# Kernel tuning notes

Hardware: AMD Instinct MI355X
Metric: run time of the kernel (lower is better)

## Reference

```python
import jax, jax.numpy as jnp
import numpy as np

B, C, E, S, L, N = 2, 256, 256, 3, 5, 128
HMAX = 128
LEVEL_SIZES = np.array([128, 64, 32, 16, 8])
STRIDES = np.array([8.0, 16.0, 32.0, 64.0, 128.0])
GROUPS = 8
EPS = 1e-5


def setup_inputs() -> dict:
    key = jax.random.key(0)
    ks = jax.random.split(key, 16)
    # Padded FPN pyramid stacked as [L, B, C, HMAX, HMAX]; level l valid in [:sz, :sz]
    fm = jnp.zeros((L, B, C, HMAX, HMAX), jnp.float32)
    for l in range(L):
        sz = int(LEVEL_SIZES[l])
        fm = fm.at[l, :, :, :sz, :sz].set(jax.random.normal(ks[l], (B, C, sz, sz), jnp.float32))
    # Boxes in 1024x1024 image coordinates (x1, y1, x2, y2)
    cxy = jax.random.uniform(ks[5], (N, 2), minval=60.0, maxval=960.0)
    wh = jax.random.uniform(ks[6], (N, 2), minval=8.0, maxval=96.0)
    boxes = jnp.concatenate([cxy - wh / 2, cxy + wh / 2], axis=1)
    batch_idx = jax.random.randint(ks[7], (N,), 0, B, jnp.int32)
    level_idx = jax.random.randint(ks[8], (N,), 0, L, jnp.int32)
    sym_ids = jax.random.randint(ks[9], (N,), 0, 6, jnp.int32)
    conv_w = jax.random.normal(ks[10], (E, C, 3, 3), jnp.float32) / np.float32(np.sqrt(C * 9))
    gn_scale = jnp.ones((E,), jnp.float32)
    gn_bias = jnp.zeros((E,), jnp.float32)
    head_w = jax.random.normal(ks[11], (E, E), jnp.float32) / np.float32(np.sqrt(E))
    head_b = jnp.zeros((E,), jnp.float32)
    spat_w = jax.random.normal(ks[12], (E, 4), jnp.float32) * 0.01
    spat_b = jnp.zeros((E,), jnp.float32)
    sym_emb = jax.random.normal(ks[13], (6, E), jnp.float32) * 0.05
    fuse_w = jax.random.normal(ks[14], (6, E, E), jnp.float32) / np.float32(np.sqrt(E))
    fuse_b = jnp.zeros((6, E), jnp.float32)
    return dict(feature_maps=fm, boxes=boxes, conv_w=conv_w, gn_scale=gn_scale,
                gn_bias=gn_bias, head_w=head_w, head_b=head_b, spat_w=spat_w,
                spat_b=spat_b, sym_emb=sym_emb, fuse_w=fuse_w, fuse_b=fuse_b,
                batch_idx=batch_idx, level_idx=level_idx, sym_ids=sym_ids)


def _roi_align(fm, boxes, batch_idx, level_idx):
    # Batched roi_align (aligned=False, sampling_ratio=1) over all boxes at once.
    scale = (1.0 / jnp.asarray(STRIDES, fm.dtype))[level_idx]          # [N]
    hv = jnp.asarray(LEVEL_SIZES, fm.dtype)[level_idx]                 # [N] valid H=W per box
    x1 = boxes[:, 0] * scale; y1 = boxes[:, 1] * scale
    x2 = boxes[:, 2] * scale; y2 = boxes[:, 3] * scale
    roi_w = jnp.maximum(x2 - x1, 1.0)
    roi_h = jnp.maximum(y2 - y1, 1.0)
    off = (jnp.arange(S, dtype=fm.dtype) + 0.5) / S                    # bin centers
    xs = x1[:, None] + off[None, :] * roi_w[:, None]                   # [N,S]
    ys = y1[:, None] + off[None, :] * roi_h[:, None]                   # [N,S]
    y = jnp.broadcast_to(ys[:, :, None], (ys.shape[0], S, S))          # [N,S,S]
    x = jnp.broadcast_to(xs[:, None, :], (xs.shape[0], S, S))
    hvb = hv[:, None, None]
    valid = (y > -1.0) & (y < hvb) & (x > -1.0) & (x < hvb)
    yc = jnp.clip(y, 0.0, hvb - 1.0)
    xc = jnp.clip(x, 0.0, hvb - 1.0)
    y0 = jnp.floor(yc).astype(jnp.int32)
    x0 = jnp.floor(xc).astype(jnp.int32)
    hi = (hvb - 1.0).astype(jnp.int32)
    y1i = jnp.minimum(y0 + 1, hi)
    x1i = jnp.minimum(x0 + 1, hi)
    ly = yc - y0.astype(fm.dtype)
    lx = xc - x0.astype(fm.dtype)
    lvl = level_idx[:, None, None]
    bix = batch_idx[:, None, None]

    def g(yi, xi):
        # gather only the 4 corner pixels -> [N,S,S,C]
        return fm[lvl, bix, :, yi, xi]

    v = ((1 - ly) * (1 - lx))[..., None] * g(y0, x0) \
      + ((1 - ly) * lx)[..., None] * g(y0, x1i) \
      + (ly * (1 - lx))[..., None] * g(y1i, x0) \
      + (ly * lx)[..., None] * g(y1i, x1i)
    v = jnp.where(valid[..., None], v, 0.0)
    return jnp.transpose(v, (0, 3, 1, 2))                              # [N,C,S,S]


def _forward(feature_maps, boxes, conv_w, gn_scale, gn_bias, head_w, head_b,
             spat_w, spat_b, sym_emb, fuse_w, fuse_b, batch_idx, level_idx, sym_ids):
    roi = _roi_align(feature_maps, boxes, batch_idx, level_idx)        # [N,C,S,S]
    h = jax.lax.conv_general_dilated(roi, conv_w, (1, 1), ((1, 1), (1, 1)),
                                     dimension_numbers=('NCHW', 'OIHW', 'NCHW'))  # [N,E,S,S]
    n = h.shape[0]
    hg = h.reshape(n, GROUPS, -1)
    mu = hg.mean(-1, keepdims=True)
    var = hg.var(-1, keepdims=True)
    hg = (hg - mu) * jax.lax.rsqrt(var + EPS)
    h = hg.reshape(h.shape) * gn_scale[None, :, None, None] + gn_bias[None, :, None, None]
    h = jax.nn.relu(h)
    h = h.reshape(n, E, -1).mean(-1)                                   # spatial mean -> [N,E]
    head_out = jax.nn.relu(h @ head_w.T + head_b)                      # sym_feat_nn + ReLU
    spat = jax.nn.relu(boxes @ spat_w.T + spat_b)                      # spatial_embeddings
    fused_in = head_out + spat + sym_emb[sym_ids]                      # + class embedding
    out = jax.nn.relu(jnp.einsum('ne,nfe->nf', fused_in, fuse_w[sym_ids]) + fuse_b[sym_ids])
    return out                                                          # [N,E]


def reference(feature_maps, boxes, conv_w, gn_scale, gn_bias, head_w, head_b,
              spat_w, spat_b, sym_emb, fuse_w, fuse_b, batch_idx, level_idx, sym_ids):
    return _forward(feature_maps, boxes, conv_w, gn_scale, gn_bias, head_w, head_b,
                    spat_w, spat_b, sym_emb, fuse_w, fuse_b, batch_idx, level_idx, sym_ids)
```

## Files before the change

kernel.cpp:

```cpp
#include <hip/hip_runtime.h>
#include <hip/hip_bf16.h>


typedef float v2f __attribute__((ext_vector_type(2)));

__device__ __forceinline__ float bf_lo(unsigned u) { return __uint_as_float(u << 16); }
__device__ __forceinline__ float bf_hi(unsigned u) { return __uint_as_float(u & 0xffff0000u); }
__device__ __forceinline__ unsigned short f2bf(float f) {
    __hip_bfloat16 h = __float2bfloat16(f);
    return *(unsigned short*)&h;
}

__global__ __launch_bounds__(256) void prep_k(
    const float* __restrict__ conv_w,
    const float* __restrict__ head_w, const float* __restrict__ fuse_w,
    const float* __restrict__ fm, const float* __restrict__ boxes,
    const int* __restrict__ batch_idx, const int* __restrict__ level_idx,
    unsigned short* __restrict__ w8, unsigned short* __restrict__ w9,
    unsigned short* __restrict__ head_wTb, unsigned short* __restrict__ fuse_wTb,
    float* __restrict__ roiT) {
    int blk = blockIdx.x;
    int t = threadIdx.x;

    if (blk < 256) {
        int c = blk, e = t;
        const float* src = conv_w + ((size_t)e * 256 + c) * 9;
        unsigned short tmp[8];
#pragma unroll
        for (int k = 0; k < 8; ++k) tmp[k] = f2bf(src[k]);
        ((uint4*)w8)[(size_t)c * 256 + e] = *(const uint4*)tmp;
        w9[(size_t)c * 256 + e] = f2bf(src[8]);
        return;
    }

    if (blk < 704) {
        __shared__ float tile[32][33];
        int q = blk - 256;
        int z = q >> 6;
        int rem = q & 63;
        int bx = (rem & 7) * 32, by = (rem >> 3) * 32;
        const float* in = (z == 0) ? head_w : fuse_w + (size_t)(z - 1) * 65536;
        unsigned short* out = (z == 0) ? head_wTb : fuse_wTb + (size_t)(z - 1) * 65536;
        int tx = t & 31, ty = t >> 5;
#pragma unroll
        for (int i = 0; i < 32; i += 8)
            tile[ty + i][tx] = in[(size_t)(by + ty + i) * 256 + bx + tx];
        __syncthreads();
#pragma unroll
        for (int i = 0; i < 32; i += 8) {
            int k = bx + ty + i;
            int e = by + tx;
            out[(size_t)((k >> 1) * 256 + e) * 2 + (k & 1)] = f2bf(tile[tx][ty + i]);
        }
        return;
    }

    {
        int q = blk - 704;
        int n = q & 127, p = q >> 7;
        int i = p / 3, j = p % 3;
        int c = t;

        int lvl = level_idx[n];
        int b = batch_idx[n];
        const float sizes[5]  = {128.f, 64.f, 32.f, 16.f, 8.f};
        const float invstr[5] = {1.f/8.f, 1.f/16.f, 1.f/32.f, 1.f/64.f, 1.f/128.f};
        float scale = invstr[lvl];
        float hv = sizes[lvl];

        float x1 = boxes[n*4+0] * scale, y1 = boxes[n*4+1] * scale;
        float x2 = boxes[n*4+2] * scale, y2 = boxes[n*4+3] * scale;
        float rw = fmaxf(x2 - x1, 1.f), rh = fmaxf(y2 - y1, 1.f);
        float x = x1 + (((float)j + 0.5f) / 3.f) * rw;
        float y = y1 + (((float)i + 0.5f) / 3.f) * rh;

        bool valid = (y > -1.f) && (y < hv) && (x > -1.f) && (x < hv);
        float yc = fminf(fmaxf(y, 0.f), hv - 1.f);
        float xc = fminf(fmaxf(x, 0.f), hv - 1.f);
        int y0 = (int)floorf(yc), x0 = (int)floorf(xc);
        int hi = (int)(hv - 1.f);
        int y1i = min(y0 + 1, hi), x1i = min(x0 + 1, hi);
        float ly = yc - (float)y0, lx = xc - (float)x0;

        const float* base = fm + (((size_t)lvl * 2 + b) * 256 + c) * (128 * 128);
        float v00 = base[y0 * 128 + x0];
        float v01 = base[y0 * 128 + x1i];
        float v10 = base[y1i * 128 + x0];
        float v11 = base[y1i * 128 + x1i];
        float v = (1.f - ly) * (1.f - lx) * v00 + (1.f - ly) * lx * v01 +
                  ly * (1.f - lx) * v10 + ly * lx * v11;
        roiT[((size_t)n * 9 + p) * 256 + c] = valid ? v : 0.f;
    }
}

__global__ __launch_bounds__(512, 2) void conv_gn_pool(
    const float* __restrict__ roiT,
    const unsigned short* __restrict__ w8, const unsigned short* __restrict__ w9,
    const float* __restrict__ gn_scale, const float* __restrict__ gn_bias,
    float* __restrict__ pooled) {
    __shared__ float redA[4 * 64 * 9];
    __shared__ float redB[4 * 64 * 9];

    int np = blockIdx.x >> 2;
    int eq = blockIdx.x & 3;
    int n0 = np * 2, n1 = n0 + 1;
    int t = threadIdx.x;
    int e_loc = t & 63;
    int ch = __builtin_amdgcn_readfirstlane(t >> 6);
    int e = eq * 64 + e_loc;

    const float* r0 = roiT + (size_t)n0 * 2304;
    const float* r1 = roiT + (size_t)n1 * 2304;

    v2f acc[9];
#pragma unroll
    for (int p = 0; p < 9; ++p) acc[p] = (v2f)(0.f);

    int c0 = ch * 32;
#pragma unroll 2
    for (int c = c0; c < c0 + 32; c += 2) {
        v2f q0[9], q1[9];
#pragma unroll
        for (int jj = 0; jj < 9; ++jj) {
            q0[jj] = *(const v2f*)(r0 + jj * 256 + c);
            q1[jj] = *(const v2f*)(r1 + jj * 256 + c);
        }
        v2f rc0[9], rc1[9];
#pragma unroll
        for (int jj = 0; jj < 9; ++jj) {
            rc0[jj].x = q0[jj].x; rc0[jj].y = q1[jj].x;
            rc1[jj].x = q0[jj].y; rc1[jj].y = q1[jj].y;
        }
#pragma unroll
        for (int cc = 0; cc < 2; ++cc) {
            const v2f* r = cc ? rc1 : rc0;
            int cw = c + cc;
            uint4 wa4 = ((const uint4*)w8)[(size_t)cw * 256 + e];
            float wv[9];
            wv[0] = bf_lo(wa4.x); wv[1] = bf_hi(wa4.x);
            wv[2] = bf_lo(wa4.y); wv[3] = bf_hi(wa4.y);
            wv[4] = bf_lo(wa4.z); wv[5] = bf_hi(wa4.z);
            wv[6] = bf_lo(wa4.w); wv[7] = bf_hi(wa4.w);
            wv[8] = bf_lo((unsigned)w9[(size_t)cw * 256 + e]);
#pragma unroll
            for (int ky = 0; ky < 3; ++ky) {
#pragma unroll
                for (int kx = 0; kx < 3; ++kx) {
                    v2f w2;
                    w2.x = wv[ky * 3 + kx]; w2.y = wv[ky * 3 + kx];
#pragma unroll
                    for (int oy = 0; oy < 3; ++oy) {
                        int iy = oy + ky - 1;
                        if (iy < 0 || iy > 2) continue;
#pragma unroll
                        for (int ox = 0; ox < 3; ++ox) {
                            int ix = ox + kx - 1;
                            if (ix < 0 || ix > 2) continue;
                            int o = oy * 3 + ox, in = iy * 3 + ix;
                            acc[o] = w2 * r[in] + acc[o];
                        }
                    }
                }
            }
        }
    }

    float acc0[9], acc1[9];
#pragma unroll
    for (int p = 0; p < 9; ++p) { acc0[p] = acc[p].x; acc1[p] = acc[p].y; }

    if (ch >= 4) {
#pragma unroll
        for (int p = 0; p < 9; ++p) {
            redA[((ch - 4) * 64 + e_loc) * 9 + p] = acc0[p];
            redB[((ch - 4) * 64 + e_loc) * 9 + p] = acc1[p];
        }
    }
    __syncthreads();
    if (ch < 4) {
#pragma unroll
        for (int p = 0; p < 9; ++p) {
            acc0[p] += redA[(ch * 64 + e_loc) * 9 + p];
            acc1[p] += redB[(ch * 64 + e_loc) * 9 + p];
        }
    }
    __syncthreads();
    if (ch >= 2 && ch < 4) {
#pragma unroll
        for (int p = 0; p < 9; ++p) {
            redA[((ch - 2) * 64 + e_loc) * 9 + p] = acc0[p];
            redB[((ch - 2) * 64 + e_loc) * 9 + p] = acc1[p];
        }
    }
    __syncthreads();
    if (ch < 2) {
#pragma unroll
        for (int p = 0; p < 9; ++p) {
            acc0[p] += redA[(ch * 64 + e_loc) * 9 + p];
            acc1[p] += redB[(ch * 64 + e_loc) * 9 + p];
        }
    }
    __syncthreads();
    if (ch == 1) {
#pragma unroll
        for (int p = 0; p < 9; ++p) redA[e_loc * 9 + p] = acc0[p];
    }
    if (ch == 0) {
#pragma unroll
        for (int p = 0; p < 9; ++p) redB[e_loc * 9 + p] = acc1[p];
    }
    __syncthreads();

    if (ch < 2) {
        float accf[9];
        int n_out;
        if (ch == 0) {
            n_out = n0;
#pragma unroll
            for (int p = 0; p < 9; ++p) accf[p] = acc0[p] + redA[e_loc * 9 + p];
        } else {
            n_out = n1;
#pragma unroll
            for (int p = 0; p < 9; ++p) accf[p] = acc1[p] + redB[e_loc * 9 + p];
        }

        float s = 0.f, sq = 0.f;
#pragma unroll
        for (int p = 0; p < 9; ++p) { s += accf[p]; sq += accf[p] * accf[p]; }
#pragma unroll
        for (int m = 16; m >= 1; m >>= 1) {
            s  += __shfl_xor(s, m, 64);
            sq += __shfl_xor(sq, m, 64);
        }
        float mean = s * (1.f / 288.f);
        float var = sq * (1.f / 288.f) - mean * mean;
        float rinv = rsqrtf(var + 1e-5f);
        float gs = gn_scale[e], gb = gn_bias[e];
        float ps = 0.f;
#pragma unroll
        for (int p = 0; p < 9; ++p) {
            float v = (accf[p] - mean) * rinv * gs + gb;
            ps += fmaxf(v, 0.f);
        }
        pooled[(size_t)n_out * 256 + e] = ps * (1.f / 9.f);
    }
}

__global__ __launch_bounds__(512) void head_fuse(
    const float* __restrict__ pooled, const float* __restrict__ boxes,
    const unsigned short* __restrict__ head_wTb, const float* __restrict__ head_b,
    const float* __restrict__ spat_w, const float* __restrict__ spat_b,
    const float* __restrict__ sym_emb,
    const unsigned short* __restrict__ fuse_wTb, const float* __restrict__ fuse_b,
    const int* __restrict__ sym_ids, float* __restrict__ out) {
    __shared__ float pl[256];
    __shared__ float part[512];
    __shared__ float fin[256];
    int n = blockIdx.x;
    int t = threadIdx.x;
    int e = t & 255;
    int kh = t >> 8;
    int sid = sym_ids[n];

    if (t < 256) pl[t] = pooled[(size_t)n * 256 + t];
    __syncthreads();

    {
        float acc = 0.f;
        const unsigned* w = (const unsigned*)head_wTb + (size_t)(kh * 64) * 256 + e;
        const float* p = pl + kh * 128;
#pragma unroll 8
        for (int kp = 0; kp < 64; ++kp) {
            unsigned u = w[kp * 256];
            acc = fmaf(p[2 * kp],     bf_lo(u), acc);
            acc = fmaf(p[2 * kp + 1], bf_hi(u), acc);
        }
        part[t] = acc;
    }
    __syncthreads();
    if (t < 256) {
        float ho = fmaxf(part[t] + part[t + 256] + head_b[t], 0.f);
        float4 sw = ((const float4*)spat_w)[t];
        float b0 = boxes[n*4+0], b1 = boxes[n*4+1], b2 = boxes[n*4+2], b3 = boxes[n*4+3];
        float sp = fmaxf(spat_b[t] + b0*sw.x + b1*sw.y + b2*sw.z + b3*sw.w, 0.f);
        fin[t] = ho + sp + sym_emb[sid * 256 + t];
    }
    __syncthreads();
    {
        float o = 0.f;
        const unsigned* w = (const unsigned*)fuse_wTb + (size_t)sid * 32768
                            + (size_t)(kh * 64) * 256 + e;
        const float* p = fin + kh * 128;
#pragma unroll 8
        for (int kp = 0; kp < 64; ++kp) {
            unsigned u = w[kp * 256];
            o = fmaf(p[2 * kp],     bf_lo(u), o);
            o = fmaf(p[2 * kp + 1], bf_hi(u), o);
        }
        part[t] = o;
    }
    __syncthreads();
    if (t < 256)
        out[(size_t)n * 256 + t] = fmaxf(part[t] + part[t + 256] + fuse_b[sid * 256 + t], 0.f);
}

extern "C" void kernel_launch(void* const* d_in, const int* in_sizes, int n_in,
                              void* d_out, int out_size, void* d_ws, size_t ws_size,
                              hipStream_t stream) {
    const float* fm      = (const float*)d_in[0];
    const float* boxes   = (const float*)d_in[1];
    const float* conv_w  = (const float*)d_in[2];
    const float* gn_s    = (const float*)d_in[3];
    const float* gn_b    = (const float*)d_in[4];
    const float* head_w  = (const float*)d_in[5];
    const float* head_b  = (const float*)d_in[6];
    const float* spat_w  = (const float*)d_in[7];
    const float* spat_b  = (const float*)d_in[8];
    const float* sym_emb = (const float*)d_in[9];
    const float* fuse_w  = (const float*)d_in[10];
    const float* fuse_b  = (const float*)d_in[11];
    const int* batch_idx = (const int*)d_in[12];
    const int* level_idx = (const int*)d_in[13];
    const int* sym_ids   = (const int*)d_in[14];
    float* outp = (float*)d_out;

    char* ws = (char*)d_ws;
    unsigned short* w8       = (unsigned short*)ws;
    unsigned short* w9       = (unsigned short*)(ws + 1048576);
    unsigned short* head_wTb = (unsigned short*)(ws + 1179648);
    unsigned short* fuse_wTb = (unsigned short*)(ws + 1310720);
    float* roiT    = (float*)(ws + 2097152);
    float* pooled  = (float*)(ws + 3276800);

    prep_k<<<1856, 256, 0, stream>>>(conv_w, head_w, fuse_w, fm, boxes,
                                     batch_idx, level_idx,
                                     w8, w9, head_wTb, fuse_wTb, roiT);
    conv_gn_pool<<<256, 512, 0, stream>>>(roiT, w8, w9, gn_s, gn_b, pooled);
    head_fuse<<<128, 512, 0, stream>>>(pooled, boxes, head_wTb, head_b, spat_w, spat_b,
                                       sym_emb, fuse_wTb, fuse_b, sym_ids, outp);
}
```

Measured before the change: 249.4 us.

## Fuse conv+GroupNorm+pool with head/fuse MLP into one per-ROI kernel

Merges the conv/GN/pool kernel and the head/fuse kernel into a single kernel with one block per ROI, so pooled features stay in shared memory instead of round-tripping through global memory and a launch is removed. The work split changes from 2 ROIs × 64 channels per block (256 blocks) to 1 ROI × all 256 output channels per block (128 blocks), with each thread packing two output channels into v2f and 4 input-channel slices reduced through LDS. This halves grid size, which may reduce GPU occupancy and weight reuse across ROIs, since each block now reads the full conv weight for a single ROI.

```diff
diff --git a/kernel.cpp b/kernel.cpp
--- a/kernel.cpp
+++ b/kernel.cpp
@@ -93,189 +93,153 @@
     }
 }
 
-__global__ __launch_bounds__(512, 2) void conv_gn_pool(
+__global__ __launch_bounds__(512, 2) void conv_gn_head(
     const float* __restrict__ roiT,
     const unsigned short* __restrict__ w8, const unsigned short* __restrict__ w9,
     const float* __restrict__ gn_scale, const float* __restrict__ gn_bias,
-    float* __restrict__ pooled) {
-    __shared__ float redA[4 * 64 * 9];
-    __shared__ float redB[4 * 64 * 9];
-
-    int np = blockIdx.x >> 2;
-    int eq = blockIdx.x & 3;
-    int n0 = np * 2, n1 = n0 + 1;
-    int t = threadIdx.x;
-    int e_loc = t & 63;
-    int ch = __builtin_amdgcn_readfirstlane(t >> 6);
-    int e = eq * 64 + e_loc;
-
-    const float* r0 = roiT + (size_t)n0 * 2304;
-    const float* r1 = roiT + (size_t)n1 * 2304;
-
-    v2f acc[9];
-#pragma unroll
-    for (int p = 0; p < 9; ++p) acc[p] = (v2f)(0.f);
-
-    int c0 = ch * 32;
-#pragma unroll 2
-    for (int c = c0; c < c0 + 32; c += 2) {
-        v2f q0[9], q1[9];
-#pragma unroll
-        for (int jj = 0; jj < 9; ++jj) {
-            q0[jj] = *(const v2f*)(r0 + jj * 256 + c);
-            q1[jj] = *(const v2f*)(r1 + jj * 256 + c);
-        }
-        v2f rc0[9], rc1[9];
-#pragma unroll
-        for (int jj = 0; jj < 9; ++jj) {
-            rc0[jj].x = q0[jj].x; rc0[jj].y = q1[jj].x;
-            rc1[jj].x = q0[jj].y; rc1[jj].y = q1[jj].y;
-        }
-#pragma unroll
-        for (int cc = 0; cc < 2; ++cc) {
-            const v2f* r = cc ? rc1 : rc0;
-            int cw = c + cc;
-            uint4 wa4 = ((const uint4*)w8)[(size_t)cw * 256 + e];
-            float wv[9];
-            wv[0] = bf_lo(wa4.x); wv[1] = bf_hi(wa4.x);
-            wv[2] = bf_lo(wa4.y); wv[3] = bf_hi(wa4.y);
-            wv[4] = bf_lo(wa4.z); wv[5] = bf_hi(wa4.z);
-            wv[6] = bf_lo(wa4.w); wv[7] = bf_hi(wa4.w);
-            wv[8] = bf_lo((unsigned)w9[(size_t)cw * 256 + e]);
-#pragma unroll
-            for (int ky = 0; ky < 3; ++ky) {
-#pragma unroll
-                for (int kx = 0; kx < 3; ++kx) {
-                    v2f w2;
-                    w2.x = wv[ky * 3 + kx]; w2.y = wv[ky * 3 + kx];
-#pragma unroll
-                    for (int oy = 0; oy < 3; ++oy) {
-                        int iy = oy + ky - 1;
-                        if (iy < 0 || iy > 2) continue;
-#pragma unroll
-                        for (int ox = 0; ox < 3; ++ox) {
-                            int ix = ox + kx - 1;
-                            if (ix < 0 || ix > 2) continue;
-                            int o = oy * 3 + ox, in = iy * 3 + ix;
-                            acc[o] = w2 * r[in] + acc[o];
-                        }
-                    }
-                }
-            }
-        }
-    }
-
-    float acc0[9], acc1[9];
-#pragma unroll
-    for (int p = 0; p < 9; ++p) { acc0[p] = acc[p].x; acc1[p] = acc[p].y; }
-
-    if (ch >= 4) {
-#pragma unroll
-        for (int p = 0; p < 9; ++p) {
-            redA[((ch - 4) * 64 + e_loc) * 9 + p] = acc0[p];
-            redB[((ch - 4) * 64 + e_loc) * 9 + p] = acc1[p];
-        }
-    }
-    __syncthreads();
-    if (ch < 4) {
-#pragma unroll
-        for (int p = 0; p < 9; ++p) {
-            acc0[p] += redA[(ch * 64 + e_loc) * 9 + p];
-            acc1[p] += redB[(ch * 64 + e_loc) * 9 + p];
-        }
-    }
-    __syncthreads();
-    if (ch >= 2 && ch < 4) {
-#pragma unroll
-        for (int p = 0; p < 9; ++p) {
-            redA[((ch - 2) * 64 + e_loc) * 9 + p] = acc0[p];
-            redB[((ch - 2) * 64 + e_loc) * 9 + p] = acc1[p];
-        }
-    }
-    __syncthreads();
-    if (ch < 2) {
-#pragma unroll
-        for (int p = 0; p < 9; ++p) {
-            acc0[p] += redA[(ch * 64 + e_loc) * 9 + p];
-            acc1[p] += redB[(ch * 64 + e_loc) * 9 + p];
-        }
-    }
-    __syncthreads();
-    if (ch == 1) {
-#pragma unroll
-        for (int p = 0; p < 9; ++p) redA[e_loc * 9 + p] = acc0[p];
-    }
-    if (ch == 0) {
-#pragma unroll
-        for (int p = 0; p < 9; ++p) redB[e_loc * 9 + p] = acc1[p];
-    }
-    __syncthreads();
-
-    if (ch < 2) {
-        float accf[9];
-        int n_out;
-        if (ch == 0) {
-            n_out = n0;
-#pragma unroll
-            for (int p = 0; p < 9; ++p) accf[p] = acc0[p] + redA[e_loc * 9 + p];
-        } else {
-            n_out = n1;
-#pragma unroll
-            for (int p = 0; p < 9; ++p) accf[p] = acc1[p] + redB[e_loc * 9 + p];
-        }
-
-        float s = 0.f, sq = 0.f;
-#pragma unroll
-        for (int p = 0; p < 9; ++p) { s += accf[p]; sq += accf[p] * accf[p]; }
-#pragma unroll
-        for (int m = 16; m >= 1; m >>= 1) {
-            s  += __shfl_xor(s, m, 64);
-            sq += __shfl_xor(sq, m, 64);
-        }
-        float mean = s * (1.f / 288.f);
-        float var = sq * (1.f / 288.f) - mean * mean;
-        float rinv = rsqrtf(var + 1e-5f);
-        float gs = gn_scale[e], gb = gn_bias[e];
-        float ps = 0.f;
-#pragma unroll
-        for (int p = 0; p < 9; ++p) {
-            float v = (accf[p] - mean) * rinv * gs + gb;
-            ps += fmaxf(v, 0.f);
-        }
-        pooled[(size_t)n_out * 256 + e] = ps * (1.f / 9.f);
-    }
-}
-
-__global__ __launch_bounds__(512) void head_fuse(
-    const float* __restrict__ pooled, const float* __restrict__ boxes,
+    const float* __restrict__ boxes,
     const unsigned short* __restrict__ head_wTb, const float* __restrict__ head_b,
     const float* __restrict__ spat_w, const float* __restrict__ spat_b,
     const float* __restrict__ sym_emb,
     const unsigned short* __restrict__ fuse_wTb, const float* __restrict__ fuse_b,
     const int* __restrict__ sym_ids, float* __restrict__ out) {
+    __shared__ v2f red[2 * 128 * 9];
     __shared__ float pl[256];
     __shared__ float part[512];
     __shared__ float fin[256];
+
     int n = blockIdx.x;
     int t = threadIdx.x;
+    int ep = t & 127;
+    int ch = __builtin_amdgcn_readfirstlane(t >> 7);
+
+    const float* r = roiT + (size_t)n * 2304;
+
+    v2f acc[9];
+#pragma unroll
+    for (int p = 0; p < 9; ++p) acc[p] = (v2f)(0.f);
+
+    int c0 = ch * 64;
+#pragma unroll 2
+    for (int c = c0; c < c0 + 64; c += 2) {
+        v2f q[9];
+#pragma unroll
+        for (int jj = 0; jj < 9; ++jj)
+            q[jj] = *(const v2f*)(r + jj * 256 + c);
+
+#pragma unroll
+        for (int cc = 0; cc < 2; ++cc) {
+            int cw = c + cc;
+            uint4 wa = ((const uint4*)w8)[(size_t)cw * 256 + ep];
+            uint4 wb = ((const uint4*)w8)[(size_t)cw * 256 + ep + 128];
+            v2f w2[9];
+            w2[0].x = bf_lo(wa.x); w2[0].y = bf_lo(wb.x);
+            w2[1].x = bf_hi(wa.x); w2[1].y = bf_hi(wb.x);
+            w2[2].x = bf_lo(wa.y); w2[2].y = bf_lo(wb.y);
+            w2[3].x = bf_hi(wa.y); w2[3].y = bf_hi(wb.y);
+            w2[4].x = bf_lo(wa.z); w2[4].y = bf_lo(wb.z);
+            w2[5].x = bf_hi(wa.z); w2[5].y = bf_hi(wb.z);
+            w2[6].x = bf_lo(wa.w); w2[6].y = bf_lo(wb.w);
+            w2[7].x = bf_hi(wa.w); w2[7].y = bf_hi(wb.w);
+            w2[8].x = bf_lo((unsigned)w9[(size_t)cw * 256 + ep]);
+            w2[8].y = bf_lo((unsigned)w9[(size_t)cw * 256 + ep + 128]);
+
+            v2f rr[9];
+#pragma unroll
+            for (int jj = 0; jj < 9; ++jj) {
+                float rv = cc ? q[jj].y : q[jj].x;
+                rr[jj].x = rv; rr[jj].y = rv;
+            }
+#pragma unroll
+            for (int ky = 0; ky < 3; ++ky) {
+#pragma unroll
+                for (int kx = 0; kx < 3; ++kx) {
+                    v2f wk = w2[ky * 3 + kx];
+#pragma unroll
+                    for (int oy = 0; oy < 3; ++oy) {
+                        int iy = oy + ky - 1;
+                        if (iy < 0 || iy > 2) continue;
+#pragma unroll
+                        for (int ox = 0; ox < 3; ++ox) {
+                            int ix = ox + kx - 1;
+                            if (ix < 0 || ix > 2) continue;
+                            int o = oy * 3 + ox, in = iy * 3 + ix;
+                            acc[o] = wk * rr[in] + acc[o];
+                        }
+                    }
+                }
+            }
+        }
+    }
+
+    if (ch >= 2) {
+#pragma unroll
+        for (int p = 0; p < 9; ++p)
+            red[((ch - 2) * 128 + ep) * 9 + p] = acc[p];
+    }
+    __syncthreads();
+    if (ch < 2) {
+#pragma unroll
+        for (int p = 0; p < 9; ++p)
+            acc[p] += red[(ch * 128 + ep) * 9 + p];
+    }
+    __syncthreads();
+    if (ch == 1) {
+#pragma unroll
+        for (int p = 0; p < 9; ++p)
+            red[ep * 9 + p] = acc[p];
+    }
+    __syncthreads();
+
+    if (ch == 0) {
+#pragma unroll
+        for (int p = 0; p < 9; ++p)
+            acc[p] += red[ep * 9 + p];
+
+        v2f s = (v2f)(0.f), sq = (v2f)(0.f);
+#pragma unroll
+        for (int p = 0; p < 9; ++p) { s += acc[p]; sq += acc[p] * acc[p]; }
+#pragma unroll
+        for (int m = 16; m >= 1; m >>= 1) {
+            s.x  += __shfl_xor(s.x,  m, 64);
+            s.y  += __shfl_xor(s.y,  m, 64);
+            sq.x += __shfl_xor(sq.x, m, 64);
+            sq.y += __shfl_xor(sq.y, m, 64);
+        }
+        float mean0 = s.x * (1.f / 288.f), mean1 = s.y * (1.f / 288.f);
+        float var0 = sq.x * (1.f / 288.f) - mean0 * mean0;
+        float var1 = sq.y * (1.f / 288.f) - mean1 * mean1;
+        float ri0 = rsqrtf(var0 + 1e-5f), ri1 = rsqrtf(var1 + 1e-5f);
+        float gs0 = gn_scale[ep],       gb0 = gn_bias[ep];
+        float gs1 = gn_scale[ep + 128], gb1 = gn_bias[ep + 128];
+        float ps0 = 0.f, ps1 = 0.f;
+#pragma unroll
+        for (int p = 0; p < 9; ++p) {
+            float v0 = (acc[p].x - mean0) * ri0 * gs0 + gb0;
+            float v1 = (acc[p].y - mean1) * ri1 * gs1 + gb1;
+            ps0 += fmaxf(v0, 0.f);
+            ps1 += fmaxf(v1, 0.f);
+        }
+        pl[ep]       = ps0 * (1.f / 9.f);
+        pl[ep + 128] = ps1 * (1.f / 9.f);
+    }
+    __syncthreads();
+
     int e = t & 255;
     int kh = t >> 8;
     int sid = sym_ids[n];
 
-    if (t < 256) pl[t] = pooled[(size_t)n * 256 + t];
-    __syncthreads();
-
     {
-        float acc = 0.f;
+        float a2 = 0.f;
         const unsigned* w = (const unsigned*)head_wTb + (size_t)(kh * 64) * 256 + e;
         const float* p = pl + kh * 128;
 #pragma unroll 8
         for (int kp = 0; kp < 64; ++kp) {
             unsigned u = w[kp * 256];
-            acc = fmaf(p[2 * kp],     bf_lo(u), acc);
-            acc = fmaf(p[2 * kp + 1], bf_hi(u), acc);
-        }
-        part[t] = acc;
+            a2 = fmaf(p[2 * kp],     bf_lo(u), a2);
+            a2 = fmaf(p[2 * kp + 1], bf_hi(u), a2);
+        }
+        part[t] = a2;
     }
     __syncthreads();
     if (t < 256) {
@@ -330,12 +294,11 @@
     unsigned short* head_wTb = (unsigned short*)(ws + 1179648);
     unsigned short* fuse_wTb = (unsigned short*)(ws + 1310720);
     float* roiT    = (float*)(ws + 2097152);
-    float* pooled  = (float*)(ws + 3276800);
 
     prep_k<<<1856, 256, 0, stream>>>(conv_w, head_w, fuse_w, fm, boxes,
                                      batch_idx, level_idx,
                                      w8, w9, head_wTb, fuse_wTb, roiT);
-    conv_gn_pool<<<256, 512, 0, stream>>>(roiT, w8, w9, gn_s, gn_b, pooled);
-    head_fuse<<<128, 512, 0, stream>>>(pooled, boxes, head_wTb, head_b, spat_w, spat_b,
-                                       sym_emb, fuse_wTb, fuse_b, sym_ids, outp);
+    conv_gn_head<<<128, 512, 0, stream>>>(roiT, w8, w9, gn_s, gn_b, boxes,
+                                          head_wTb, head_b, spat_w, spat_b,
+                                          sym_emb, fuse_wTb, fuse_b, sym_ids, outp);
 }
```

Result: slower. 257.3 us (+3.2%).
